# Performance work log

Hardware: AMD Instinct MI355X
Metric: run time of the kernel (lower is better)

## Reference

```python
import jax, jax.numpy as jnp
import numpy as np

NUM_HEADS = 8

def _proj(x, W, b):
    # 1x1 conv == per-pixel linear: x [b,c,h,w], W [c_out,c_in], b [c_out]
    return jnp.einsum('bchw,oc->bohw', x, W) + b[None, :, None, None]

def setup_inputs() -> dict:
    key = jax.random.key(0)
    ks = jax.random.split(key, 5)
    b, c, h, w = 2, 256, 64, 64
    s = 0.02
    return {
        'x1': jax.random.normal(ks[0], (b, c, h, w), jnp.float32),
        'Wq': jax.random.normal(ks[1], (c, c), jnp.float32) * s,
        'bq': jnp.zeros((c,), jnp.float32),
        'Wk': jax.random.normal(ks[2], (c, c), jnp.float32) * s,
        'bk': jnp.zeros((c,), jnp.float32),
        'Wv': jax.random.normal(ks[3], (c, c), jnp.float32) * s,
        'bv': jnp.zeros((c,), jnp.float32),
        'Wo': jax.random.normal(ks[4], (c, c), jnp.float32) * s,
        'bo': jnp.zeros((c,), jnp.float32),
    }

def reference(x1, Wq, bq, Wk, bk, Wv, bv, Wo, bo):
    b, c, h, w = x1.shape
    H = NUM_HEADS
    d = c // H
    n = h * w
    scale = d ** -0.5

    def to_heads(t):
        # [b,c,h,w] -> 'b c h w -> b (h w) c' -> 'b n (H d) -> b H n d'
        # channel order: head index is the outer factor of c
        return t.reshape(b, H, d, n).transpose(0, 1, 3, 2)  # [b,H,n,d]

    q = to_heads(_proj(x1, Wq, bq))
    k = to_heads(_proj(x1, Wk, bk))
    v = to_heads(_proj(x1, Wv, bv))

    attn = jnp.einsum('bhnd,bhmd->bhnm', q, k) * scale  # [b,H,n,n]
    attn = jax.nn.softmax(attn, axis=-1)
    out = jnp.einsum('bhnm,bhmd->bhnd', attn, v)        # [b,H,n,d]
    # 'b H n d -> b n (H d)' -> 'b (h w) c -> b c h w'
    out = out.transpose(0, 2, 1, 3).reshape(b, n, c).transpose(0, 2, 1).reshape(b, c, h, w)
    return _proj(out, Wo, bo)
```

## Files before the change

### kernel.cpp

```cpp
#include <hip/hip_runtime.h>
#include <cmath>


typedef unsigned int u32;
typedef unsigned short u16;
typedef __attribute__((ext_vector_type(4))) float f32x4;
typedef __attribute__((ext_vector_type(16))) float f32x16;
typedef __attribute__((ext_vector_type(8))) short short8;
typedef __attribute__((ext_vector_type(4))) u32 u32x4;

__device__ __forceinline__ u32 cvtpk_bf16(float a, float b) {
  u32 r; asm("v_cvt_pk_bf16_f32 %0, %1, %2" : "=v"(r) : "v"(a), "v"(b)); return r;
}
__device__ __forceinline__ void pl32swap(u32 &a, u32 &b) {
  asm("v_permlane32_swap_b32 %0, %1" : "+v"(a), "+v"(b));
}
__device__ __forceinline__ u16 f2bf(float x) { return (u16)cvtpk_bf16(x, x); }

__device__ __forceinline__ f32x16 mfma16(short8 a, short8 b, f32x16 c) {
  return __builtin_amdgcn_mfma_f32_32x32x16_bf16(a, b, c, 0, 0, 0);
}

__device__ __forceinline__ void split2(float a, float b, u32 &hw, u32 &lw) {
  u32 ua = __builtin_bit_cast(u32, a), ub = __builtin_bit_cast(u32, b);
  hw = (ua >> 16) | (ub & 0xffff0000u);
  float ra = a - __builtin_bit_cast(float, ua & 0xffff0000u);
  float rb = b - __builtin_bit_cast(float, ub & 0xffff0000u);
  lw = cvtpk_bf16(ra, rb);
}
__device__ __forceinline__ void split8(f32x4 a, f32x4 b, short8 &hf, short8 &lf) {
  u32 h0,l0,h1,l1,h2,l2,h3,l3;
  split2(a[0],a[1],h0,l0); split2(a[2],a[3],h1,l1);
  split2(b[0],b[1],h2,l2); split2(b[2],b[3],h3,l3);
  u32x4 hv = {h0,h1,h2,h3}, lv = {l0,l1,l2,l3};
  hf = __builtin_bit_cast(short8, hv);
  lf = __builtin_bit_cast(short8, lv);
}

__device__ __forceinline__ int rowmap(int r, int hi) {
  return (r & 3) + 8 * ((r >> 2) & 1) + 4 * hi + 16 * (r >> 3);
}

#define QMUL (0.17677669529663689f * 1.4426950408889634f)
#define WPLANE 65536
#define WMAT  131072

__global__ __launch_bounds__(256) void prep_kernel(
    const float* __restrict__ X,
    const float* __restrict__ Wq, const float* __restrict__ Wk,
    const float* __restrict__ Wv, const float* __restrict__ Wo,
    u16* __restrict__ Xa, u16* __restrict__ Wpk)
{
  const int bx = blockIdx.x, tid = threadIdx.x;
  if (bx < 256) {
    __shared__ float lt[32 * 257];
    const int b = bx >> 7, ntile = bx & 127, n0 = ntile * 32;
    const int nn = tid & 31, cg = tid >> 5;
    #pragma unroll 4
    for (int i = 0; i < 32; i++) {
      int c = i * 8 + cg;
      lt[nn * 257 + c] = X[((size_t)b * 256 + c) * 4096 + n0 + nn];
    }
    __syncthreads();
    const int lane = tid & 63, w = tid >> 6;
    const int l31 = lane & 31, fh = lane >> 5;
    #pragma unroll
    for (int kk = 0; kk < 4; kk++) {
      int kt = w * 4 + kk;
      const float* p = &lt[l31 * 257 + kt * 16 + fh * 8];
      u32x4 pk = { cvtpk_bf16(p[0],p[1]), cvtpk_bf16(p[2],p[3]),
                   cvtpk_bf16(p[4],p[5]), cvtpk_bf16(p[6],p[7]) };
      *(u32x4*)(&Xa[(((size_t)b * 128 + ntile) * 16 + kt) * 512 + lane * 8]) = pk;
    }
  } else {
    const int j = (bx - 256) * 256 + tid;
    const int lane = j & 63, ct = (j >> 6) & 7, kt = (j >> 9) & 15, mat = j >> 13;
    const float* W = mat == 0 ? Wq : (mat == 1 ? Wk : (mat == 2 ? Wv : Wo));
    const int c = ct * 32 + (lane & 31);
    const int k0 = kt * 16 + (lane >> 5) * 8;
    f32x4 a = *(const f32x4*)(W + (size_t)c * 256 + k0);
    f32x4 b = *(const f32x4*)(W + (size_t)c * 256 + k0 + 4);
    if (mat == 0) {
      #pragma unroll
      for (int i = 0; i < 4; i++) { a[i] *= QMUL; b[i] *= QMUL; }
    }
    short8 wh, wl; split8(a, b, wh, wl);
    size_t base = ((size_t)mat * 2) * WPLANE + ((size_t)kt * 8 + ct) * 512 + lane * 8;
    *(short8*)(&Wpk[base]) = wh;
    *(short8*)(&Wpk[base + WPLANE]) = wl;
  }
}

__global__ __launch_bounds__(256) void qkv_kernel(
    const u16* __restrict__ Xa, const u16* __restrict__ Wpk,
    const float* __restrict__ bq, const float* __restrict__ bk,
    const float* __restrict__ bv,
    u16* __restrict__ Qf, u16* __restrict__ Kf, u16* __restrict__ V3)
{
  const int z = blockIdx.z, mode = z % 3, b = z / 3;
  const int tid = threadIdx.x, lane = tid & 63, wv = tid >> 6;
  const int wn = wv & 1, wcH = wv >> 1;
  const int ntile = blockIdx.x * 2 + wn;
  const int l31 = lane & 31, fh = lane >> 5;

  const u16* Amat = Xa + ((size_t)b * 128 + ntile) * 8192;
  const u16* Bmat = Wpk + (size_t)mode * WMAT;

  f32x16 acc[4] = {{}, {}, {}, {}};
  for (int kt = 0; kt < 16; kt++) {
    short8 xa = *(const short8*)(Amat + kt * 512 + lane * 8);
    #pragma unroll
    for (int i = 0; i < 4; i++) {
      int ct = wcH * 4 + i;
      const u16* wp = Bmat + ((size_t)kt * 8 + ct) * 512 + lane * 8;
      short8 wh = *(const short8*)(wp);
      short8 wl = *(const short8*)(wp + WPLANE);
      acc[i] = mfma16(wh, xa, acc[i]);
      acc[i] = mfma16(wl, xa, acc[i]);
    }
  }

  const float* bias = mode == 0 ? bq : (mode == 1 ? bk : bv);
  const float bscale = mode == 0 ? QMUL : 1.0f;

  if (mode == 2) {
    #pragma unroll
    for (int i = 0; i < 4; i++) {
      int head = wcH * 4 + i;
      size_t tb = (((size_t)(b * 8 + head) * 128 + ntile) * 32) * 32;
      #pragma unroll
      for (int r = 0; r < 16; r++) {
        int dv = rowmap(r, fh);
        V3[tb + (size_t)dv * 32 + l31] = f2bf(acc[i][r] + bias[head * 32 + dv]);
      }
    }
  } else {
    u16* Out = mode == 0 ? Qf : Kf;
    #pragma unroll
    for (int i = 0; i < 4; i++) {
      int head = wcH * 4 + i;
      size_t nb = (((size_t)(b * 8 + head) * 128 + ntile) * 2) * 512;
      #pragma unroll
      for (int kt2 = 0; kt2 < 2; kt2++) {
        float v[8];
        #pragma unroll
        for (int e = 0; e < 8; e++) {
          int c = head * 32 + rowmap(kt2 * 8 + e, fh);
          v[e] = acc[i][kt2 * 8 + e] + bscale * bias[c];
        }
        u32x4 pk = { cvtpk_bf16(v[0],v[1]), cvtpk_bf16(v[2],v[3]),
                     cvtpk_bf16(v[4],v[5]), cvtpk_bf16(v[6],v[7]) };
        *(u32x4*)(&Out[nb + (size_t)kt2 * 512 + lane * 8]) = pk;
      }
    }
  }
}

__global__ __launch_bounds__(256, 4) void attn_kernel(
    const u16* __restrict__ Qf, const u16* __restrict__ Kf,
    const u16* __restrict__ V3, u16* __restrict__ OaH, u16* __restrict__ OaL)
{
  const int fid = blockIdx.x;
  const int xcd = fid & 7, j = fid >> 3;
  const int bh = xcd + 8 * (j >> 6);
  const int qgrp = j & 63;
  const int b = bh >> 3, h = bh & 7;

  const int tid = threadIdx.x, wv = tid >> 6, lane = tid & 63;
  const int l31 = lane & 31, fh = lane >> 5;

  const u16* qfb = Qf + (size_t)bh * 131072 + (size_t)(qgrp * 2) * 1024 + lane * 8;
  short8 qa0 = *(const short8*)(qfb);
  short8 qa1 = *(const short8*)(qfb + 512);
  short8 qb0 = *(const short8*)(qfb + 1024);
  short8 qb1 = *(const short8*)(qfb + 1536);

  const u16* kfb = Kf + (size_t)bh * 131072;
  const u16* vfb = V3 + (size_t)bh * 131072;

  f32x16 accA = {}, accB = {};
  float lsA0 = 0.f, lsA1 = 0.f, lsB0 = 0.f, lsB1 = 0.f;

  int kvt = wv * 32;
  short8 kc0 = *(const short8*)(kfb + (size_t)kvt * 1024 + lane * 8);
  short8 kc1 = *(const short8*)(kfb + (size_t)kvt * 1024 + 512 + lane * 8);
  short8 vc0 = *(const short8*)(vfb + (size_t)kvt * 1024 + l31 * 32 + fh * 8);
  short8 vc1 = *(const short8*)(vfb + (size_t)kvt * 1024 + l31 * 32 + fh * 8 + 16);

  for (int it = 0; it < 32; it++) {
    int nx = wv * 32 + ((it + 1) & 31);
    const u16* kpn = kfb + (size_t)nx * 1024 + lane * 8;
    const u16* vpn = vfb + (size_t)nx * 1024 + l31 * 32 + fh * 8;
    short8 kn0 = *(const short8*)(kpn);
    short8 kn1 = *(const short8*)(kpn + 512);
    short8 vn0 = *(const short8*)(vpn);
    short8 vn1 = *(const short8*)(vpn + 16);

    {
      f32x16 s = {};
      s = mfma16(kc0, qa0, s);
      s = mfma16(kc1, qa1, s);
      #pragma unroll
      for (int r = 0; r < 16; r++) s[r] = __builtin_amdgcn_exp2f(s[r]);
      lsA0 += (s[0]+s[1]) + (s[4]+s[5]);
      lsA1 += (s[2]+s[3]) + (s[6]+s[7]);
      lsA0 += (s[8]+s[9]) + (s[12]+s[13]);
      lsA1 += (s[10]+s[11]) + (s[14]+s[15]);
      u32 a0 = cvtpk_bf16(s[0],s[1]),   b0 = cvtpk_bf16(s[4],s[5]);
      u32 c1 = cvtpk_bf16(s[2],s[3]),   d1 = cvtpk_bf16(s[6],s[7]);
      u32 e0 = cvtpk_bf16(s[8],s[9]),   f0 = cvtpk_bf16(s[12],s[13]);
      u32 g1 = cvtpk_bf16(s[10],s[11]), h1 = cvtpk_bf16(s[14],s[15]);
      pl32swap(a0,b0); pl32swap(c1,d1); pl32swap(e0,f0); pl32swap(g1,h1);
      u32x4 u0 = {a0,c1,b0,d1}, u1 = {e0,g1,f0,h1};
      accA = mfma16(__builtin_bit_cast(short8,u0), vc0, accA);
      accA = mfma16(__builtin_bit_cast(short8,u1), vc1, accA);
    }
    {
      f32x16 s = {};
      s = mfma16(kc0, qb0, s);
      s = mfma16(kc1, qb1, s);
      #pragma unroll
      for (int r = 0; r < 16; r++) s[r] = __builtin_amdgcn_exp2f(s[r]);
      lsB0 += (s[0]+s[1]) + (s[4]+s[5]);
      lsB1 += (s[2]+s[3]) + (s[6]+s[7]);
      lsB0 += (s[8]+s[9]) + (s[12]+s[13]);
      lsB1 += (s[10]+s[11]) + (s[14]+s[15]);
      u32 a0 = cvtpk_bf16(s[0],s[1]),   b0 = cvtpk_bf16(s[4],s[5]);
      u32 c1 = cvtpk_bf16(s[2],s[3]),   d1 = cvtpk_bf16(s[6],s[7]);
      u32 e0 = cvtpk_bf16(s[8],s[9]),   f0 = cvtpk_bf16(s[12],s[13]);
      u32 g1 = cvtpk_bf16(s[10],s[11]), h1 = cvtpk_bf16(s[14],s[15]);
      pl32swap(a0,b0); pl32swap(c1,d1); pl32swap(e0,f0); pl32swap(g1,h1);
      u32x4 u0 = {a0,c1,b0,d1}, u1 = {e0,g1,f0,h1};
      accB = mfma16(__builtin_bit_cast(short8,u0), vc0, accB);
      accB = mfma16(__builtin_bit_cast(short8,u1), vc1, accB);
    }
    kc0 = kn0; kc1 = kn1; vc0 = vn0; vc1 = vn1;
  }

  __shared__ float accbA[4][64][17], accbB[4][64][17];
  __shared__ float lsb2[2][4][64];

  lsb2[0][wv][lane] = lsA0 + lsA1;
  lsb2[1][wv][lane] = lsB0 + lsB1;
  #pragma unroll
  for (int r = 0; r < 16; r++) { accbA[wv][lane][r] = accA[r]; accbB[wv][lane][r] = accB[r]; }
  __syncthreads();

  const int set = wv & 1, kt = wv >> 1;
  const int qp = l31;
  float Lt = 0.f;
  #pragma unroll
  for (int w2 = 0; w2 < 4; w2++) Lt += lsb2[set][w2][qp] + lsb2[set][w2][qp + 32];
  const float Linv = 1.0f / Lt;

  const int hi_w = (qp >> 2) & 1;
  const int rr = (qp & 3) + ((qp >> 3) << 2);
  float o[8];
  #pragma unroll
  for (int e = 0; e < 8; e++) {
    int idx = (kt * 16 + fh * 8 + e) + 32 * hi_w;
    float v = set ? (accbB[0][idx][rr] + accbB[1][idx][rr] + accbB[2][idx][rr] + accbB[3][idx][rr])
                  : (accbA[0][idx][rr] + accbA[1][idx][rr] + accbA[2][idx][rr] + accbA[3][idx][rr]);
    o[e] = v * Linv;
  }
  f32x4 o0 = {o[0], o[1], o[2], o[3]}, o1 = {o[4], o[5], o[6], o[7]};
  short8 oh, ol; split8(o0, o1, oh, ol);
  const int qt = qgrp * 2 + set, ktg = h * 2 + kt;
  size_t addr = (((size_t)b * 128 + qt) * 16 + ktg) * 512 + lane * 8;
  *(short8*)(&OaH[addr]) = oh;
  *(short8*)(&OaL[addr]) = ol;
}

__global__ __launch_bounds__(256) void oproj_kernel(
    const u16* __restrict__ OaH, const u16* __restrict__ OaL,
    const u16* __restrict__ Wpk, const float* __restrict__ bo,
    float* __restrict__ Out)
{
  const int b = blockIdx.z, ct = blockIdx.y;
  const int tid = threadIdx.x, lane = tid & 63, wv = tid >> 6;
  const int ntile = blockIdx.x * 4 + wv;
  const int l31 = lane & 31, fh = lane >> 5;

  const u16* Wo = Wpk + (size_t)3 * WMAT;
  const u16* Ob = OaH + ((size_t)b * 128 + ntile) * 8192;
  const u16* Ol = OaL + ((size_t)b * 128 + ntile) * 8192;

  f32x16 acc = {};
  for (int kt = 0; kt < 16; kt++) {
    const u16* wp = Wo + ((size_t)kt * 8 + ct) * 512 + lane * 8;
    short8 wh = *(const short8*)(wp);
    short8 wl = *(const short8*)(wp + WPLANE);
    short8 oh = *(const short8*)(Ob + kt * 512 + lane * 8);
    short8 ol = *(const short8*)(Ol + kt * 512 + lane * 8);
    acc = mfma16(wh, oh, acc);
    acc = mfma16(wh, ol, acc);
    acc = mfma16(wl, oh, acc);
  }
  #pragma unroll
  for (int r = 0; r < 16; r++) {
    int c = ct * 32 + rowmap(r, fh);
    Out[((size_t)b * 256 + c) * 4096 + ntile * 32 + l31] = acc[r] + bo[c];
  }
}

extern "C" void kernel_launch(void* const* d_in, const int* in_sizes, int n_in,
                              void* d_out, int out_size, void* d_ws, size_t ws_size,
                              hipStream_t stream) {
  const float* x1 = (const float*)d_in[0];
  const float* Wq = (const float*)d_in[1];
  const float* bq = (const float*)d_in[2];
  const float* Wk = (const float*)d_in[3];
  const float* bk = (const float*)d_in[4];
  const float* Wv = (const float*)d_in[5];
  const float* bv = (const float*)d_in[6];
  const float* Wo = (const float*)d_in[7];
  const float* bo = (const float*)d_in[8];

  const size_t NEL = (size_t)2 * 4096 * 256;
  u16* Xa  = (u16*)d_ws;
  u16* Qf  = Xa + NEL;
  u16* Kf  = Qf + NEL;
  u16* V3  = Kf + NEL;
  u16* OaL = V3 + NEL;
  u16* Wpk = OaL + NEL;
  u16* OaH = Xa;
  float* out = (float*)d_out;

  prep_kernel<<<dim3(384), 256, 0, stream>>>(x1, Wq, Wk, Wv, Wo, Xa, Wpk);
  qkv_kernel<<<dim3(64, 1, 6), 256, 0, stream>>>(Xa, Wpk, bq, bk, bv, Qf, Kf, V3);
  attn_kernel<<<dim3(1024), 256, 0, stream>>>(Qf, Kf, V3, OaH, OaL);
  oproj_kernel<<<dim3(32, 8, 2), 256, 0, stream>>>(OaH, OaL, Wpk, bo, out);
}
```

Baseline: 148.1 us.

## Permute V layout to drop permlane swaps, compute row sums via MFMA

The V tiles are now written with a key-index permutation (tau) so that the exp'd score fragments can feed the PV MFMA directly as the B operand, with V as the A operand. This removes the v_permlane32_swap shuffles. Softmax row sums are now accumulated by extra MFMAs against a ones vector instead of scalar adds, and the hand-written K/V register prefetch is dropped. The QKV projection grid is doubled with each wave covering fewer column tiles, and attention launch bounds go from 4 to 3 occupancy. The trade-off is extra MFMA work and the loss of explicit load/compute overlap.

```diff
diff --git a/kernel.cpp b/kernel.cpp
--- a/kernel.cpp
+++ b/kernel.cpp
@@ -11,9 +11,6 @@
 
 __device__ __forceinline__ u32 cvtpk_bf16(float a, float b) {
   u32 r; asm("v_cvt_pk_bf16_f32 %0, %1, %2" : "=v"(r) : "v"(a), "v"(b)); return r;
-}
-__device__ __forceinline__ void pl32swap(u32 &a, u32 &b) {
-  asm("v_permlane32_swap_b32 %0, %1" : "+v"(a), "+v"(b));
 }
 __device__ __forceinline__ u16 f2bf(float x) { return (u16)cvtpk_bf16(x, x); }
 
@@ -39,6 +36,9 @@
 
 __device__ __forceinline__ int rowmap(int r, int hi) {
   return (r & 3) + 8 * ((r >> 2) & 1) + 4 * hi + 16 * (r >> 3);
+}
+__device__ __forceinline__ int tau(int kv) {
+  return (kv & 19) | ((kv & 4) << 1) | ((kv & 8) >> 1);
 }
 
 #define QMUL (0.17677669529663689f * 1.4426950408889634f)
@@ -99,19 +99,18 @@
 {
   const int z = blockIdx.z, mode = z % 3, b = z / 3;
   const int tid = threadIdx.x, lane = tid & 63, wv = tid >> 6;
-  const int wn = wv & 1, wcH = wv >> 1;
-  const int ntile = blockIdx.x * 2 + wn;
+  const int ntile = blockIdx.x;
   const int l31 = lane & 31, fh = lane >> 5;
 
   const u16* Amat = Xa + ((size_t)b * 128 + ntile) * 8192;
   const u16* Bmat = Wpk + (size_t)mode * WMAT;
 
-  f32x16 acc[4] = {{}, {}, {}, {}};
+  f32x16 acc[2] = {{}, {}};
   for (int kt = 0; kt < 16; kt++) {
     short8 xa = *(const short8*)(Amat + kt * 512 + lane * 8);
     #pragma unroll
-    for (int i = 0; i < 4; i++) {
-      int ct = wcH * 4 + i;
+    for (int i = 0; i < 2; i++) {
+      int ct = wv * 2 + i;
       const u16* wp = Bmat + ((size_t)kt * 8 + ct) * 512 + lane * 8;
       short8 wh = *(const short8*)(wp);
       short8 wl = *(const short8*)(wp + WPLANE);
@@ -124,22 +123,23 @@
   const float bscale = mode == 0 ? QMUL : 1.0f;
 
   if (mode == 2) {
-    #pragma unroll
-    for (int i = 0; i < 4; i++) {
-      int head = wcH * 4 + i;
-      size_t tb = (((size_t)(b * 8 + head) * 128 + ntile) * 32) * 32;
+    const int sl = tau(l31);
+    #pragma unroll
+    for (int i = 0; i < 2; i++) {
+      int head = wv * 2 + i;
+      size_t tb = ((size_t)(b * 8 + head) * 128 + ntile) * 1024;
       #pragma unroll
       for (int r = 0; r < 16; r++) {
         int dv = rowmap(r, fh);
-        V3[tb + (size_t)dv * 32 + l31] = f2bf(acc[i][r] + bias[head * 32 + dv]);
+        V3[tb + (size_t)dv * 32 + sl] = f2bf(acc[i][r] + bias[head * 32 + dv]);
       }
     }
   } else {
     u16* Out = mode == 0 ? Qf : Kf;
     #pragma unroll
-    for (int i = 0; i < 4; i++) {
-      int head = wcH * 4 + i;
-      size_t nb = (((size_t)(b * 8 + head) * 128 + ntile) * 2) * 512;
+    for (int i = 0; i < 2; i++) {
+      int head = wv * 2 + i;
+      size_t nb = ((size_t)(b * 8 + head) * 128 + ntile) * 1024;
       #pragma unroll
       for (int kt2 = 0; kt2 < 2; kt2++) {
         float v[8];
@@ -156,7 +156,7 @@
   }
 }
 
-__global__ __launch_bounds__(256, 4) void attn_kernel(
+__global__ __launch_bounds__(256, 3) void attn_kernel(
     const u16* __restrict__ Qf, const u16* __restrict__ Kf,
     const u16* __restrict__ V3, u16* __restrict__ OaH, u16* __restrict__ OaL)
 {
@@ -178,94 +178,79 @@
   const u16* kfb = Kf + (size_t)bh * 131072;
   const u16* vfb = V3 + (size_t)bh * 131072;
 
-  f32x16 accA = {}, accB = {};
-  float lsA0 = 0.f, lsA1 = 0.f, lsB0 = 0.f, lsB1 = 0.f;
-
-  int kvt = wv * 32;
-  short8 kc0 = *(const short8*)(kfb + (size_t)kvt * 1024 + lane * 8);
-  short8 kc1 = *(const short8*)(kfb + (size_t)kvt * 1024 + 512 + lane * 8);
-  short8 vc0 = *(const short8*)(vfb + (size_t)kvt * 1024 + l31 * 32 + fh * 8);
-  short8 vc1 = *(const short8*)(vfb + (size_t)kvt * 1024 + l31 * 32 + fh * 8 + 16);
+  const u32x4 onesu = {0x3F803F80u, 0x3F803F80u, 0x3F803F80u, 0x3F803F80u};
+  const short8 ones = __builtin_bit_cast(short8, onesu);
+
+  f32x16 accA = {}, accB = {}, sumA = {}, sumB = {};
 
   for (int it = 0; it < 32; it++) {
-    int nx = wv * 32 + ((it + 1) & 31);
-    const u16* kpn = kfb + (size_t)nx * 1024 + lane * 8;
-    const u16* vpn = vfb + (size_t)nx * 1024 + l31 * 32 + fh * 8;
-    short8 kn0 = *(const short8*)(kpn);
-    short8 kn1 = *(const short8*)(kpn + 512);
-    short8 vn0 = *(const short8*)(vpn);
-    short8 vn1 = *(const short8*)(vpn + 16);
-
-    {
-      f32x16 s = {};
-      s = mfma16(kc0, qa0, s);
-      s = mfma16(kc1, qa1, s);
-      #pragma unroll
-      for (int r = 0; r < 16; r++) s[r] = __builtin_amdgcn_exp2f(s[r]);
-      lsA0 += (s[0]+s[1]) + (s[4]+s[5]);
-      lsA1 += (s[2]+s[3]) + (s[6]+s[7]);
-      lsA0 += (s[8]+s[9]) + (s[12]+s[13]);
-      lsA1 += (s[10]+s[11]) + (s[14]+s[15]);
-      u32 a0 = cvtpk_bf16(s[0],s[1]),   b0 = cvtpk_bf16(s[4],s[5]);
-      u32 c1 = cvtpk_bf16(s[2],s[3]),   d1 = cvtpk_bf16(s[6],s[7]);
-      u32 e0 = cvtpk_bf16(s[8],s[9]),   f0 = cvtpk_bf16(s[12],s[13]);
-      u32 g1 = cvtpk_bf16(s[10],s[11]), h1 = cvtpk_bf16(s[14],s[15]);
-      pl32swap(a0,b0); pl32swap(c1,d1); pl32swap(e0,f0); pl32swap(g1,h1);
-      u32x4 u0 = {a0,c1,b0,d1}, u1 = {e0,g1,f0,h1};
-      accA = mfma16(__builtin_bit_cast(short8,u0), vc0, accA);
-      accA = mfma16(__builtin_bit_cast(short8,u1), vc1, accA);
-    }
-    {
-      f32x16 s = {};
-      s = mfma16(kc0, qb0, s);
-      s = mfma16(kc1, qb1, s);
-      #pragma unroll
-      for (int r = 0; r < 16; r++) s[r] = __builtin_amdgcn_exp2f(s[r]);
-      lsB0 += (s[0]+s[1]) + (s[4]+s[5]);
-      lsB1 += (s[2]+s[3]) + (s[6]+s[7]);
-      lsB0 += (s[8]+s[9]) + (s[12]+s[13]);
-      lsB1 += (s[10]+s[11]) + (s[14]+s[15]);
-      u32 a0 = cvtpk_bf16(s[0],s[1]),   b0 = cvtpk_bf16(s[4],s[5]);
-      u32 c1 = cvtpk_bf16(s[2],s[3]),   d1 = cvtpk_bf16(s[6],s[7]);
-      u32 e0 = cvtpk_bf16(s[8],s[9]),   f0 = cvtpk_bf16(s[12],s[13]);
-      u32 g1 = cvtpk_bf16(s[10],s[11]), h1 = cvtpk_bf16(s[14],s[15]);
-      pl32swap(a0,b0); pl32swap(c1,d1); pl32swap(e0,f0); pl32swap(g1,h1);
-      u32x4 u0 = {a0,c1,b0,d1}, u1 = {e0,g1,f0,h1};
-      accB = mfma16(__builtin_bit_cast(short8,u0), vc0, accB);
-      accB = mfma16(__builtin_bit_cast(short8,u1), vc1, accB);
-    }
-    kc0 = kn0; kc1 = kn1; vc0 = vn0; vc1 = vn1;
-  }
-
-  __shared__ float accbA[4][64][17], accbB[4][64][17];
-  __shared__ float lsb2[2][4][64];
-
-  lsb2[0][wv][lane] = lsA0 + lsA1;
-  lsb2[1][wv][lane] = lsB0 + lsB1;
+    const int kvt = wv * 32 + it;
+    const u16* kp = kfb + (size_t)kvt * 1024 + lane * 8;
+    const u16* vp = vfb + (size_t)kvt * 1024 + l31 * 32 + fh * 8;
+    short8 kc0 = *(const short8*)(kp);
+    short8 kc1 = *(const short8*)(kp + 512);
+    short8 vc0 = *(const short8*)(vp);
+    short8 vc1 = *(const short8*)(vp + 16);
+
+    f32x16 sA = {}, sB = {};
+    sA = mfma16(kc0, qa0, sA);
+    sA = mfma16(kc1, qa1, sA);
+    sB = mfma16(kc0, qb0, sB);
+    sB = mfma16(kc1, qb1, sB);
+
+    #pragma unroll
+    for (int r = 0; r < 16; r++) sA[r] = __builtin_amdgcn_exp2f(sA[r]);
+    u32x4 uA0 = { cvtpk_bf16(sA[0],sA[1]),  cvtpk_bf16(sA[2],sA[3]),
+                  cvtpk_bf16(sA[4],sA[5]),  cvtpk_bf16(sA[6],sA[7]) };
+    u32x4 uA1 = { cvtpk_bf16(sA[8],sA[9]),  cvtpk_bf16(sA[10],sA[11]),
+                  cvtpk_bf16(sA[12],sA[13]),cvtpk_bf16(sA[14],sA[15]) };
+    short8 pA0 = __builtin_bit_cast(short8, uA0);
+    short8 pA1 = __builtin_bit_cast(short8, uA1);
+    accA = mfma16(vc0, pA0, accA);
+    accA = mfma16(vc1, pA1, accA);
+    sumA = mfma16(ones, pA0, sumA);
+    sumA = mfma16(ones, pA1, sumA);
+
+    #pragma unroll
+    for (int r = 0; r < 16; r++) sB[r] = __builtin_amdgcn_exp2f(sB[r]);
+    u32x4 uB0 = { cvtpk_bf16(sB[0],sB[1]),  cvtpk_bf16(sB[2],sB[3]),
+                  cvtpk_bf16(sB[4],sB[5]),  cvtpk_bf16(sB[6],sB[7]) };
+    u32x4 uB1 = { cvtpk_bf16(sB[8],sB[9]),  cvtpk_bf16(sB[10],sB[11]),
+                  cvtpk_bf16(sB[12],sB[13]),cvtpk_bf16(sB[14],sB[15]) };
+    short8 pB0 = __builtin_bit_cast(short8, uB0);
+    short8 pB1 = __builtin_bit_cast(short8, uB1);
+    accB = mfma16(vc0, pB0, accB);
+    accB = mfma16(vc1, pB1, accB);
+    sumB = mfma16(ones, pB0, sumB);
+    sumB = mfma16(ones, pB1, sumB);
+  }
+
+  __shared__ float accb[2][4][64][17];
+  __shared__ float lsb[2][4][64];
+
   #pragma unroll
-  for (int r = 0; r < 16; r++) { accbA[wv][lane][r] = accA[r]; accbB[wv][lane][r] = accB[r]; }
+  for (int r = 0; r < 16; r++) { accb[0][wv][lane][r] = accA[r]; accb[1][wv][lane][r] = accB[r]; }
+  lsb[0][wv][lane] = sumA[0];
+  lsb[1][wv][lane] = sumB[0];
   __syncthreads();
 
-  const int set = wv & 1, kt = wv >> 1;
-  const int qp = l31;
-  float Lt = 0.f;
-  #pragma unroll
-  for (int w2 = 0; w2 < 4; w2++) Lt += lsb2[set][w2][qp] + lsb2[set][w2][qp + 32];
+  const int set = wv & 1, ktl = wv >> 1;
+  const float Lt = (lsb[set][0][l31] + lsb[set][1][l31]) +
+                   (lsb[set][2][l31] + lsb[set][3][l31]);
   const float Linv = 1.0f / Lt;
 
-  const int hi_w = (qp >> 2) & 1;
-  const int rr = (qp & 3) + ((qp >> 3) << 2);
   float o[8];
   #pragma unroll
   for (int e = 0; e < 8; e++) {
-    int idx = (kt * 16 + fh * 8 + e) + 32 * hi_w;
-    float v = set ? (accbB[0][idx][rr] + accbB[1][idx][rr] + accbB[2][idx][rr] + accbB[3][idx][rr])
-                  : (accbA[0][idx][rr] + accbA[1][idx][rr] + accbA[2][idx][rr] + accbA[3][idx][rr]);
-    o[e] = v * Linv;
+    int hs = (e >> 2) & 1;
+    int r = (e & 3) + 4 * fh + 8 * ktl;
+    int li = hs * 32 + l31;
+    o[e] = Linv * ((accb[set][0][li][r] + accb[set][1][li][r]) +
+                   (accb[set][2][li][r] + accb[set][3][li][r]));
   }
   f32x4 o0 = {o[0], o[1], o[2], o[3]}, o1 = {o[4], o[5], o[6], o[7]};
   short8 oh, ol; split8(o0, o1, oh, ol);
-  const int qt = qgrp * 2 + set, ktg = h * 2 + kt;
+  const int qt = qgrp * 2 + set, ktg = h * 2 + ktl;
   size_t addr = (((size_t)b * 128 + qt) * 16 + ktg) * 512 + lane * 8;
   *(short8*)(&OaH[addr]) = oh;
   *(short8*)(&OaL[addr]) = ol;
@@ -327,7 +312,7 @@
   float* out = (float*)d_out;
 
   prep_kernel<<<dim3(384), 256, 0, stream>>>(x1, Wq, Wk, Wv, Wo, Xa, Wpk);
-  qkv_kernel<<<dim3(64, 1, 6), 256, 0, stream>>>(Xa, Wpk, bq, bk, bv, Qf, Kf, V3);
+  qkv_kernel<<<dim3(128, 1, 6), 256, 0, stream>>>(Xa, Wpk, bq, bk, bv, Qf, Kf, V3);
   attn_kernel<<<dim3(1024), 256, 0, stream>>>(Qf, Kf, V3, OaH, OaL);
   oproj_kernel<<<dim3(32, 8, 2), 256, 0, stream>>>(OaH, OaL, Wpk, bo, out);
 }
```

Result: faster. 140.8 us (-4.9%).
